# Kernel optimization log

Hardware: AMD Instinct MI355X
Metric: run time of the kernel (lower is better)

## Reference

```python
import jax, jax.numpy as jnp
import numpy as np

B, S, D, C = 64, 576, 768, 200


def setup_inputs() -> dict:
    key = jax.random.key(0)
    k1, k2, k3, k4 = jax.random.split(key, 4)
    return {
        "patch_tokens": jax.random.normal(k1, (B, S, D), dtype=jnp.float32),
        "class_token": jax.random.normal(k2, (B, D), dtype=jnp.float32),
        "attn_w": jax.random.normal(k3, (C, D), dtype=jnp.float32) * (1.0 / np.sqrt(D)),
        "attn_b": jnp.zeros((C,), dtype=jnp.float32),
        "gc_w": jax.random.normal(k4, (C, D), dtype=jnp.float32) * (1.0 / np.sqrt(D)),
        "gc_b": jnp.zeros((C,), dtype=jnp.float32),
        "lam": jnp.ones((1,), dtype=jnp.float32),
    }


def reference(patch_tokens, class_token, attn_w, attn_b, gc_w, gc_b, lam):
    # patch_tokens: (B,S,D). The torch module reshapes S to HxW, but the mean
    # over (H,W) equals the mean over S, so we stay in token layout.
    _, S_, D_ = patch_tokens.shape
    # Global classifier: (B,C)
    global_scores = class_token @ gc_w.T + gc_b
    # Per-class 1x1 conv == per-class linear projection over tokens: (B,C,S)
    att = jax.nn.sigmoid(
        jnp.einsum("bsd,cd->bcs", patch_tokens, attn_w) + attn_b[None, :, None]
    )
    # mean over spatial (S) then mean over channels (D):
    # mean_d mean_s (att * feat) == einsum / (S*D)
    attention_scores = jnp.einsum("bcs,bsd->bc", att, patch_tokens) / (S_ * D_)
    return global_scores + lam[0] * attention_scores
```

## Files before the change

kernel.cpp:

```cpp
#include <hip/hip_runtime.h>
#include <math.h>

#define Bsz  64
#define Ssz  576
#define Dsz  768
#define Csz  200
#define NPAD 208
#define MT   32
#define NKT  12

typedef short short8 __attribute__((ext_vector_type(8)));
typedef float f32x4  __attribute__((ext_vector_type(4)));

__device__ inline unsigned short f2bf_rne(float f) {
    union { float f; unsigned int u; } v; v.f = f;
    return (unsigned short)((v.u + 0x7FFFu + ((v.u >> 16) & 1u)) >> 16);
}
__device__ inline unsigned int pack2bf(float lo, float hi) {
    union { float f; unsigned int u; } a, b; a.f = lo; b.f = hi;
    return __builtin_amdgcn_perm(b.u + 0x8000u, a.u + 0x8000u, 0x07060302u);
}

__global__ __launch_bounds__(256) void prep_w(const float* __restrict__ W,
                                              unsigned short* __restrict__ Wb) {
    const int i   = blockIdx.x * 256 + threadIdx.x;
    const int row = i / (Dsz / 4);
    const int col = (i % (Dsz / 4)) * 4;
    ushort4 h;
    if (row < Csz) {
        const float4 v = *(const float4*)(W + (size_t)row * Dsz + col);
        h.x = f2bf_rne(v.x); h.y = f2bf_rne(v.y); h.z = f2bf_rne(v.z); h.w = f2bf_rne(v.w);
    } else if (row == Csz) {
        h.x = h.y = h.z = h.w = 0x3F80;
    } else {
        h.x = h.y = h.z = h.w = 0;
    }
    *(ushort4*)(Wb + (size_t)row * Dsz + col) = h;
}

__global__ __launch_bounds__(256) void gc_kernel(
    const float* __restrict__ ct, const float* __restrict__ gw,
    const float* __restrict__ gb, float* __restrict__ out) {
    const int b    = blockIdx.x;
    const int wv   = threadIdx.x >> 6;
    const int lane = threadIdx.x & 63;
    const int c    = blockIdx.y * 4 + wv;
    const float* wr = gw + (size_t)c * Dsz + lane * 12;
    const float* cr = ct + (size_t)b * Dsz + lane * 12;
    float s = 0.f;
#pragma unroll
    for (int j = 0; j < 3; ++j) {
        const float4 w = *(const float4*)(wr + 4 * j);
        const float4 x = *(const float4*)(cr + 4 * j);
        s += w.x * x.x + w.y * x.y + w.z * x.z + w.w * x.w;
    }
#pragma unroll
    for (int off = 32; off > 0; off >>= 1) s += __shfl_down(s, off, 64);
    if (lane == 0) out[b * Csz + c] = s + gb[c];
}

__global__ __launch_bounds__(64, 2) void attn_kernel(
    const float* __restrict__ X,
    const unsigned short* __restrict__ Wb,
    const float* __restrict__ attn_b,
    const float* __restrict__ lam,
    float* __restrict__ out)
{
    const int lane = threadIdx.x;
    const int m = lane & 15;
    const int q = lane >> 4;
    const int rowbase = blockIdx.x * MT;
    const int bidx    = rowbase / Ssz;

    f32x4 acc0[13], acc1[13];
#pragma unroll
    for (int t = 0; t < 13; ++t) {
        acc0[t] = (f32x4){0.f, 0.f, 0.f, 0.f};
        acc1[t] = (f32x4){0.f, 0.f, 0.f, 0.f};
    }

    const float* xp0 = X + (size_t)(rowbase + m) * Dsz + q * 8;
    const float* xp1 = xp0 + 16 * Dsz;
    const unsigned short* wp = Wb + (size_t)m * Dsz + q * 8;

    float4 c0[4], c1[4];
    c0[0] = *(const float4*)(xp0);      c0[1] = *(const float4*)(xp0 + 4);
    c0[2] = *(const float4*)(xp0 + 32); c0[3] = *(const float4*)(xp0 + 36);
    c1[0] = *(const float4*)(xp1);      c1[1] = *(const float4*)(xp1 + 4);
    c1[2] = *(const float4*)(xp1 + 32); c1[3] = *(const float4*)(xp1 + 36);

    for (int kt = 0; kt < NKT; ++kt) {
        const int kn = (kt + 1 < NKT) ? (kt + 1) * 64 : kt * 64;
        float4 n0[4], n1[4];
        n0[0] = *(const float4*)(xp0 + kn);      n0[1] = *(const float4*)(xp0 + kn + 4);
        n0[2] = *(const float4*)(xp0 + kn + 32); n0[3] = *(const float4*)(xp0 + kn + 36);
        n1[0] = *(const float4*)(xp1 + kn);      n1[1] = *(const float4*)(xp1 + kn + 4);
        n1[2] = *(const float4*)(xp1 + kn + 32); n1[3] = *(const float4*)(xp1 + kn + 36);

        union { short8 s; unsigned int u[4]; } a00, a01, a10, a11;
        a00.u[0] = pack2bf(c0[0].x, c0[0].y); a00.u[1] = pack2bf(c0[0].z, c0[0].w);
        a00.u[2] = pack2bf(c0[1].x, c0[1].y); a00.u[3] = pack2bf(c0[1].z, c0[1].w);
        a01.u[0] = pack2bf(c0[2].x, c0[2].y); a01.u[1] = pack2bf(c0[2].z, c0[2].w);
        a01.u[2] = pack2bf(c0[3].x, c0[3].y); a01.u[3] = pack2bf(c0[3].z, c0[3].w);
        a10.u[0] = pack2bf(c1[0].x, c1[0].y); a10.u[1] = pack2bf(c1[0].z, c1[0].w);
        a10.u[2] = pack2bf(c1[1].x, c1[1].y); a10.u[3] = pack2bf(c1[1].z, c1[1].w);
        a11.u[0] = pack2bf(c1[2].x, c1[2].y); a11.u[1] = pack2bf(c1[2].z, c1[2].w);
        a11.u[2] = pack2bf(c1[3].x, c1[3].y); a11.u[3] = pack2bf(c1[3].z, c1[3].w);

        const unsigned short* wk = wp + kt * 64;
#pragma unroll
        for (int t = 0; t < 13; ++t) {
            const short8 b0 = *(const short8*)(wk + (size_t)t * 16 * Dsz);
            acc0[t] = __builtin_amdgcn_mfma_f32_16x16x32_bf16(a00.s, b0, acc0[t], 0, 0, 0);
            acc1[t] = __builtin_amdgcn_mfma_f32_16x16x32_bf16(a10.s, b0, acc1[t], 0, 0, 0);
        }
#pragma unroll
        for (int t = 0; t < 13; ++t) {
            const short8 b1 = *(const short8*)(wk + (size_t)t * 16 * Dsz + 32);
            acc0[t] = __builtin_amdgcn_mfma_f32_16x16x32_bf16(a01.s, b1, acc0[t], 0, 0, 0);
            acc1[t] = __builtin_amdgcn_mfma_f32_16x16x32_bf16(a11.s, b1, acc1[t], 0, 0, 0);
        }
#pragma unroll
        for (int j = 0; j < 4; ++j) { c0[j] = n0[j]; c1[j] = n1[j]; }
    }

    float rs0[4], rs1[4];
#pragma unroll
    for (int r = 0; r < 4; ++r) {
        rs0[r] = __shfl(acc0[12][r], (lane & 48) + 8, 64);
        rs1[r] = __shfl(acc1[12][r], (lane & 48) + 8, 64);
    }
    const float scale = lam[0] * (1.f / ((float)Ssz * (float)Dsz));

#pragma unroll
    for (int t = 0; t < 13; ++t) {
        const int c = t * 16 + m;
        if (c < Csz) {
            const float bias = attn_b[c];
            float s = 0.f;
#pragma unroll
            for (int r = 0; r < 4; ++r) {
                s += rs0[r] / (1.f + __expf(-(acc0[t][r] + bias)));
                s += rs1[r] / (1.f + __expf(-(acc1[t][r] + bias)));
            }
            s += __shfl_xor(s, 16, 64);
            s += __shfl_xor(s, 32, 64);
            if (q == 0) atomicAdd(&out[bidx * Csz + c], s * scale);
        }
    }
}

extern "C" void kernel_launch(void* const* d_in, const int* in_sizes, int n_in,
                              void* d_out, int out_size, void* d_ws, size_t ws_size,
                              hipStream_t stream) {
    const float* X   = (const float*)d_in[0];
    const float* ct  = (const float*)d_in[1];
    const float* aw  = (const float*)d_in[2];
    const float* ab  = (const float*)d_in[3];
    const float* gw  = (const float*)d_in[4];
    const float* gb  = (const float*)d_in[5];
    const float* lam = (const float*)d_in[6];
    float* out = (float*)d_out;
    unsigned short* Wb = (unsigned short*)d_ws;

    prep_w<<<(NPAD * Dsz / 4) / 256, 256, 0, stream>>>(aw, Wb);
    gc_kernel<<<dim3(Bsz, Csz / 4), 256, 0, stream>>>(ct, gw, gb, out);
    attn_kernel<<<(Bsz * Ssz) / MT, 64, 0, stream>>>(X, Wb, ab, lam, out);
}
```

Measured before the change: 230.1 us.

## Split attention GEMM tile across four waves and compute row sums directly

The attention kernel moves from one 64-thread wave per 32-row tile to four waves per block. Each wave handles 16 rows and about half of the 13 class tiles, which cuts accumulator registers per wave and raises occupancy. The token row-sum used for weighting was previously produced by an extra MFMA tile against a row of ones in the padded weight. It is now accumulated in fp32 from the loaded values and reduced with shuffles, so prep_w no longer writes the ones row. The cost is that each X row is loaded twice, once by each wave in a pair, and the grid issues more atomics per output.

```diff
diff --git a/kernel.cpp b/kernel.cpp
--- a/kernel.cpp
+++ b/kernel.cpp
@@ -26,14 +26,10 @@
     const int i   = blockIdx.x * 256 + threadIdx.x;
     const int row = i / (Dsz / 4);
     const int col = (i % (Dsz / 4)) * 4;
-    ushort4 h;
+    ushort4 h = {0, 0, 0, 0};
     if (row < Csz) {
         const float4 v = *(const float4*)(W + (size_t)row * Dsz + col);
         h.x = f2bf_rne(v.x); h.y = f2bf_rne(v.y); h.z = f2bf_rne(v.z); h.w = f2bf_rne(v.w);
-    } else if (row == Csz) {
-        h.x = h.y = h.z = h.w = 0x3F80;
-    } else {
-        h.x = h.y = h.z = h.w = 0;
     }
     *(ushort4*)(Wb + (size_t)row * Dsz + col) = h;
 }
@@ -59,93 +55,93 @@
     if (lane == 0) out[b * Csz + c] = s + gb[c];
 }
 
-__global__ __launch_bounds__(64, 2) void attn_kernel(
+__global__ __launch_bounds__(256, 4) void attn_kernel(
     const float* __restrict__ X,
     const unsigned short* __restrict__ Wb,
     const float* __restrict__ attn_b,
     const float* __restrict__ lam,
     float* __restrict__ out)
 {
-    const int lane = threadIdx.x;
-    const int m = lane & 15;
-    const int q = lane >> 4;
+    const int tid  = threadIdx.x;
+    const int lane = tid & 63;
+    const int w    = tid >> 6;
+    const int g    = w >> 1;
+    const int h    = w & 1;
+    const int m    = lane & 15;
+    const int q    = lane >> 4;
+    const int NT   = h ? 6 : 7;
+    const int t0   = h * 7;
     const int rowbase = blockIdx.x * MT;
     const int bidx    = rowbase / Ssz;
 
-    f32x4 acc0[13], acc1[13];
+    f32x4 acc[7];
 #pragma unroll
-    for (int t = 0; t < 13; ++t) {
-        acc0[t] = (f32x4){0.f, 0.f, 0.f, 0.f};
-        acc1[t] = (f32x4){0.f, 0.f, 0.f, 0.f};
+    for (int t = 0; t < 7; ++t) acc[t] = (f32x4){0.f, 0.f, 0.f, 0.f};
+
+    const float* xp = X + (size_t)(rowbase + g * 16 + m) * Dsz + q * 8;
+    const unsigned short* wp = Wb + (size_t)m * Dsz + q * 8;
+
+    float4 c0 = *(const float4*)(xp);
+    float4 c1 = *(const float4*)(xp + 4);
+    float4 c2 = *(const float4*)(xp + 32);
+    float4 c3 = *(const float4*)(xp + 36);
+    float rs = 0.f;
+
+    for (int kt = 0; kt < NKT; ++kt) {
+        const int kn = ((kt + 1 < NKT) ? kt + 1 : kt) * 64;
+        float4 n0 = *(const float4*)(xp + kn);
+        float4 n1 = *(const float4*)(xp + kn + 4);
+        float4 n2 = *(const float4*)(xp + kn + 32);
+        float4 n3 = *(const float4*)(xp + kn + 36);
+
+        union { short8 s; unsigned int u[4]; } a0, a1;
+        a0.u[0] = pack2bf(c0.x, c0.y); a0.u[1] = pack2bf(c0.z, c0.w);
+        a0.u[2] = pack2bf(c1.x, c1.y); a0.u[3] = pack2bf(c1.z, c1.w);
+        a1.u[0] = pack2bf(c2.x, c2.y); a1.u[1] = pack2bf(c2.z, c2.w);
+        a1.u[2] = pack2bf(c3.x, c3.y); a1.u[3] = pack2bf(c3.z, c3.w);
+        rs += (c0.x + c0.y + c0.z + c0.w) + (c1.x + c1.y + c1.z + c1.w)
+            + (c2.x + c2.y + c2.z + c2.w) + (c3.x + c3.y + c3.z + c3.w);
+
+        const unsigned short* wk = wp + kt * 64;
+        short8 b0[7], b1[7];
+#pragma unroll
+        for (int t = 0; t < 7; ++t)
+            if (t < NT) b0[t] = *(const short8*)(wk + (size_t)(t0 + t) * 16 * Dsz);
+#pragma unroll
+        for (int t = 0; t < 7; ++t)
+            if (t < NT) b1[t] = *(const short8*)(wk + (size_t)(t0 + t) * 16 * Dsz + 32);
+#pragma unroll
+        for (int t = 0; t < 7; ++t)
+            if (t < NT) acc[t] = __builtin_amdgcn_mfma_f32_16x16x32_bf16(a0.s, b0[t], acc[t], 0, 0, 0);
+#pragma unroll
+        for (int t = 0; t < 7; ++t)
+            if (t < NT) acc[t] = __builtin_amdgcn_mfma_f32_16x16x32_bf16(a1.s, b1[t], acc[t], 0, 0, 0);
+
+        c0 = n0; c1 = n1; c2 = n2; c3 = n3;
     }
 
-    const float* xp0 = X + (size_t)(rowbase + m) * Dsz + q * 8;
-    const float* xp1 = xp0 + 16 * Dsz;
-    const unsigned short* wp = Wb + (size_t)m * Dsz + q * 8;
+    rs += __shfl_xor(rs, 16, 64);
+    rs += __shfl_xor(rs, 32, 64);
+    float rsv[4];
+#pragma unroll
+    for (int r = 0; r < 4; ++r) rsv[r] = __shfl(rs, q * 4 + r, 64);
 
-    float4 c0[4], c1[4];
-    c0[0] = *(const float4*)(xp0);      c0[1] = *(const float4*)(xp0 + 4);
-    c0[2] = *(const float4*)(xp0 + 32); c0[3] = *(const float4*)(xp0 + 36);
-    c1[0] = *(const float4*)(xp1);      c1[1] = *(const float4*)(xp1 + 4);
-    c1[2] = *(const float4*)(xp1 + 32); c1[3] = *(const float4*)(xp1 + 36);
-
-    for (int kt = 0; kt < NKT; ++kt) {
-        const int kn = (kt + 1 < NKT) ? (kt + 1) * 64 : kt * 64;
-        float4 n0[4], n1[4];
-        n0[0] = *(const float4*)(xp0 + kn);      n0[1] = *(const float4*)(xp0 + kn + 4);
-        n0[2] = *(const float4*)(xp0 + kn + 32); n0[3] = *(const float4*)(xp0 + kn + 36);
-        n1[0] = *(const float4*)(xp1 + kn);      n1[1] = *(const float4*)(xp1 + kn + 4);
-        n1[2] = *(const float4*)(xp1 + kn + 32); n1[3] = *(const float4*)(xp1 + kn + 36);
-
-        union { short8 s; unsigned int u[4]; } a00, a01, a10, a11;
-        a00.u[0] = pack2bf(c0[0].x, c0[0].y); a00.u[1] = pack2bf(c0[0].z, c0[0].w);
-        a00.u[2] = pack2bf(c0[1].x, c0[1].y); a00.u[3] = pack2bf(c0[1].z, c0[1].w);
-        a01.u[0] = pack2bf(c0[2].x, c0[2].y); a01.u[1] = pack2bf(c0[2].z, c0[2].w);
-        a01.u[2] = pack2bf(c0[3].x, c0[3].y); a01.u[3] = pack2bf(c0[3].z, c0[3].w);
-        a10.u[0] = pack2bf(c1[0].x, c1[0].y); a10.u[1] = pack2bf(c1[0].z, c1[0].w);
-        a10.u[2] = pack2bf(c1[1].x, c1[1].y); a10.u[3] = pack2bf(c1[1].z, c1[1].w);
-        a11.u[0] = pack2bf(c1[2].x, c1[2].y); a11.u[1] = pack2bf(c1[2].z, c1[2].w);
-        a11.u[2] = pack2bf(c1[3].x, c1[3].y); a11.u[3] = pack2bf(c1[3].z, c1[3].w);
-
-        const unsigned short* wk = wp + kt * 64;
-#pragma unroll
-        for (int t = 0; t < 13; ++t) {
-            const short8 b0 = *(const short8*)(wk + (size_t)t * 16 * Dsz);
-            acc0[t] = __builtin_amdgcn_mfma_f32_16x16x32_bf16(a00.s, b0, acc0[t], 0, 0, 0);
-            acc1[t] = __builtin_amdgcn_mfma_f32_16x16x32_bf16(a10.s, b0, acc1[t], 0, 0, 0);
-        }
-#pragma unroll
-        for (int t = 0; t < 13; ++t) {
-            const short8 b1 = *(const short8*)(wk + (size_t)t * 16 * Dsz + 32);
-            acc0[t] = __builtin_amdgcn_mfma_f32_16x16x32_bf16(a01.s, b1, acc0[t], 0, 0, 0);
-            acc1[t] = __builtin_amdgcn_mfma_f32_16x16x32_bf16(a11.s, b1, acc1[t], 0, 0, 0);
-        }
-#pragma unroll
-        for (int j = 0; j < 4; ++j) { c0[j] = n0[j]; c1[j] = n1[j]; }
-    }
-
-    float rs0[4], rs1[4];
-#pragma unroll
-    for (int r = 0; r < 4; ++r) {
-        rs0[r] = __shfl(acc0[12][r], (lane & 48) + 8, 64);
-        rs1[r] = __shfl(acc1[12][r], (lane & 48) + 8, 64);
-    }
     const float scale = lam[0] * (1.f / ((float)Ssz * (float)Dsz));
 
 #pragma unroll
-    for (int t = 0; t < 13; ++t) {
-        const int c = t * 16 + m;
-        if (c < Csz) {
-            const float bias = attn_b[c];
-            float s = 0.f;
+    for (int t = 0; t < 7; ++t) {
+        if (t < NT) {
+            const int c = (t0 + t) * 16 + m;
+            if (c < Csz) {
+                const float bias = attn_b[c];
+                float s = 0.f;
 #pragma unroll
-            for (int r = 0; r < 4; ++r) {
-                s += rs0[r] / (1.f + __expf(-(acc0[t][r] + bias)));
-                s += rs1[r] / (1.f + __expf(-(acc1[t][r] + bias)));
+                for (int r = 0; r < 4; ++r)
+                    s += rsv[r] / (1.f + __expf(-(acc[t][r] + bias)));
+                s += __shfl_xor(s, 16, 64);
+                s += __shfl_xor(s, 32, 64);
+                if (q == 0) atomicAdd(&out[bidx * Csz + c], s * scale);
             }
-            s += __shfl_xor(s, 16, 64);
-            s += __shfl_xor(s, 32, 64);
-            if (q == 0) atomicAdd(&out[bidx * Csz + c], s * scale);
         }
     }
 }
@@ -165,5 +161,5 @@
 
     prep_w<<<(NPAD * Dsz / 4) / 256, 256, 0, stream>>>(aw, Wb);
     gc_kernel<<<dim3(Bsz, Csz / 4), 256, 0, stream>>>(ct, gw, gb, out);
-    attn_kernel<<<(Bsz * Ssz) / MT, 64, 0, stream>>>(X, Wb, ab, lam, out);
+    attn_kernel<<<(Bsz * Ssz) / MT, 256, 0, stream>>>(X, Wb, ab, lam, out);
 }
```

Result: slower. 271.2 us (+17.9%).
